# Kernel tuning notes

Measured on AMD Instinct MI355X. Metric: run time of the kernel, lower is better.

The kernel has to match this reference:

```python
import jax, jax.numpy as jnp
import numpy as np

B, S, D = 4, 1024, 768
H = 12
DK = D // H            # 64
NUM_EMB = 10
MAX_DIST = 100000.0 * 2 ** 0.5
POS_SCALE = 100000.0   # tile positions live in [0, 100000]


def setup_inputs() -> dict:
    key = jax.random.key(0)
    ks = jax.random.split(key, 12)
    query = jax.random.normal(ks[0], (B, S, D), dtype=jnp.float32)
    key_t = jax.random.normal(ks[1], (B, S, D), dtype=jnp.float32)
    value = jax.random.normal(ks[2], (B, S, D), dtype=jnp.float32)
    tile_positions = jax.random.uniform(ks[3], (B, S, 2), dtype=jnp.float32) * POS_SCALE
    # Linear weights, torch layout [out, in]; xavier_uniform init, zero bias
    lim = float(np.sqrt(6.0 / (D + D)))
    Wq = jax.random.uniform(ks[4], (D, D), minval=-lim, maxval=lim, dtype=jnp.float32)
    Wk = jax.random.uniform(ks[5], (D, D), minval=-lim, maxval=lim, dtype=jnp.float32)
    Wv = jax.random.uniform(ks[6], (D, D), minval=-lim, maxval=lim, dtype=jnp.float32)
    bq = jnp.zeros((D,), jnp.float32)
    bk = jnp.zeros((D,), jnp.float32)
    bv = jnp.zeros((D,), jnp.float32)
    emb_k = jax.random.normal(ks[7], (NUM_EMB, DK), dtype=jnp.float32)  # nn.Embedding default N(0,1)
    return {"query": query, "key": key_t, "value": value,
            "tile_positions": tile_positions,
            "Wq": Wq, "bq": bq, "Wk": Wk, "bk": bk, "Wv": Wv, "bv": bv,
            "emb_k": emb_k}


def reference(query, key, value, tile_positions, Wq, bq, Wk, bk, Wv, bv, emb_k):
    b, s, _ = query.shape
    # projections -> [B, H, S, DK]
    q = (query @ Wq.T + bq).reshape(b, s, H, DK).transpose(0, 2, 1, 3)
    k = (key   @ Wk.T + bk).reshape(b, s, H, DK).transpose(0, 2, 1, 3)
    v = (value @ Wv.T + bv).reshape(b, s, H, DK).transpose(0, 2, 1, 3)
    # pairwise distances, normalized, discretized to embedding indices
    pos = jax.lax.stop_gradient(tile_positions)
    diff = pos[:, :, None, :] - pos[:, None, :, :]          # [B,S,S,2]
    dist = jnp.sqrt(jnp.sum(diff * diff, axis=-1)) / MAX_DIST  # [B,S,S]
    idx = jnp.clip(jnp.round(dist * (NUM_EMB - 1)), 0, NUM_EMB - 1).astype(jnp.int32)
    rk = emb_k[idx]                                          # [B,S,S,DK]
    # logits: QK^T plus distance-aware key bias
    attn_logits = jnp.einsum('bhqd,bhkd->bhqk', q, k)
    attn_logits = attn_logits + jnp.einsum('bhqd,bqkd->bhqk', q, rk)
    attn_logits = attn_logits / (DK ** 0.5)
    attention = jax.nn.softmax(attn_logits, axis=-1)
    out = jnp.einsum('bhqk,bhkd->bhqd', attention, v)       # [B,H,S,DK]
    out = out.transpose(0, 2, 1, 3).reshape(b, s, -1)       # [B,S,D]
    return out
```

## Files before the change

### kernel.cpp

```cpp
#include <hip/hip_runtime.h>
#include <hip/hip_bf16.h>

#define Bsz 4
#define Ssz 1024
#define Dsz 768
#define Hn 12
#define DKsz 64
#define NUMEMB 10

#define IDX_OFF 64
#define K_OFF   4194368
#define V_OFF   10485824
#define WBF_OFF 16777280
#define XBF_OFF 20316224
#define WS_TIER_B 20316224ULL
#define WS_TIER_A 39190592ULL

#define NXz 3145728
#define NWz 589824

#define QE_RS 12
#define QE_QS 776

typedef __attribute__((ext_vector_type(8))) short short8;
typedef __attribute__((ext_vector_type(8))) float float8;
typedef __attribute__((ext_vector_type(4))) float f32x4;
typedef __attribute__((ext_vector_type(4))) unsigned int u32x4;
typedef __attribute__((ext_vector_type(2))) unsigned int u32x2;
typedef __attribute__((ext_vector_type(4))) short s16x4;

__device__ __forceinline__ float bfbits2f(short u) {
    union { unsigned int i; float f; } v;
    v.i = ((unsigned int)(unsigned short)u) << 16;
    return v.f;
}
__device__ __forceinline__ unsigned short f2bf_bits(float f) {
    __hip_bfloat16 h = __float2bfloat16(f);
    return *reinterpret_cast<unsigned short*>(&h);
}

__device__ __forceinline__ void gld16(const short* g, short* l) {
    __builtin_amdgcn_global_load_lds(
        (const __attribute__((address_space(1))) void*)g,
        (__attribute__((address_space(3))) void*)l, 16, 0, 0);
}

template<bool BF16>
__device__ __forceinline__ float loadf(const void* base, size_t idx) {
    if constexpr (BF16) return __bfloat162float(((const __hip_bfloat16*)base)[idx]);
    else return ((const float*)base)[idx];
}
template<bool BF16>
__device__ __forceinline__ short8 load8bf(const void* base, size_t idx) {
    if constexpr (BF16) {
        return *(const short8*)((const short*)base + idx);
    } else {
        float8 f = *(const float8*)((const float*)base + idx);
        short8 r;
#pragma unroll
        for (int i = 0; i < 8; i++) r[i] = (short)f2bf_bits(f[i]);
        return r;
    }
}
template<bool BF16>
__device__ __forceinline__ float8 load8f(const void* base, size_t idx) {
    if constexpr (BF16) {
        short8 s = *(const short8*)((const short*)base + idx);
        float8 f;
#pragma unroll
        for (int i = 0; i < 8; i++) f[i] = bfbits2f(s[i]);
        return f;
    } else {
        return *(const float8*)((const float*)base + idx);
    }
}

__global__ __launch_bounds__(64) void detect_kernel(
    const unsigned int* __restrict__ q, const unsigned int* __restrict__ p,
    const unsigned int* __restrict__ w, const unsigned int* __restrict__ e,
    int* __restrict__ flags)
{
    const int which = blockIdx.x;
    const unsigned int* ptr = (which == 0) ? q : ((which == 1) ? p : ((which == 2) ? w : e));
    const int n = (which == 3) ? 320 : ((which == 1) ? 4096 : 1024);
    int cnt = 0;
    for (int i = threadIdx.x; i < n; i += 64) {
        const unsigned int ex = (ptr[i] >> 7) & 0xFF;
        cnt += (ex >= 110 && ex <= 145) ? 1 : 0;
    }
#pragma unroll
    for (int off = 1; off < 64; off <<= 1) cnt += __shfl_xor(cnt, off, 64);
    if (threadIdx.x == 0) flags[which] = (2 * cnt > n) ? 1 : 0;
}

__global__ __launch_bounds__(256) void conv_kernel(
    const void* __restrict__ X0, const void* __restrict__ X1, const void* __restrict__ X2,
    const void* __restrict__ W0, const void* __restrict__ W1, const void* __restrict__ W2,
    const int* __restrict__ flags, short* __restrict__ Xbf, short* __restrict__ Wbf,
    int doX)
{
    const long t = (long)blockIdx.x * 256 + threadIdx.x;
    const bool xb = flags[0] != 0, wb = flags[2] != 0;
    if (doX) {
        const long i8 = t * 8;
        if (i8 < (long)3 * NXz) {
            const int z = (int)(i8 / NXz);
            const long off = i8 - (long)z * NXz;
            const void* X = (z == 0) ? X0 : ((z == 1) ? X1 : X2);
            short8 v = xb ? load8bf<true>(X, off) : load8bf<false>(X, off);
            *(short8*)(Xbf + i8) = v;
        } else {
            const long j = i8 - (long)3 * NXz;
            const int z = (int)(j / NWz);
            const long off = j - (long)z * NWz;
            const void* W = (z == 0) ? W0 : ((z == 1) ? W1 : W2);
            short8 v = wb ? load8bf<true>(W, off) : load8bf<false>(W, off);
            *(short8*)(Wbf + j) = v;
        }
    } else {
        const long j = t * 8;
        const int z = (int)(j / NWz);
        const long off = j - (long)z * NWz;
        const void* W = (z == 0) ? W0 : ((z == 1) ? W1 : W2);
        short8 v = wb ? load8bf<true>(W, off) : load8bf<false>(W, off);
        *(short8*)(Wbf + j) = v;
    }
}

template<bool PB>
__device__ __forceinline__ void idx_body(
    const void* pos, unsigned char* __restrict__ idxb)
{
    const int kt = blockIdx.x, qt = blockIdx.y, b = blockIdx.z;
    const int t = threadIdx.x;
    const int r = t >> 2, cc = t & 3;
    const int q = qt * 64 + r;
    const float qx = loadf<PB>(pos, ((size_t)b * Ssz + q) * 2);
    const float qy = loadf<PB>(pos, ((size_t)b * Ssz + q) * 2 + 1);
    const float MAXD = 141421.35623730951f;
    const int k0 = kt * 64 + cc * 16;
    unsigned int w[4];
#pragma unroll
    for (int g = 0; g < 4; g++) {
        unsigned int acc = 0;
#pragma unroll
        for (int u = 0; u < 4; u++) {
            const int k = k0 + g * 4 + u;
            const float kx = loadf<PB>(pos, ((size_t)b * Ssz + k) * 2);
            const float ky = loadf<PB>(pos, ((size_t)b * Ssz + k) * 2 + 1);
            const float dx = __fsub_rn(qx, kx);
            const float dy = __fsub_rn(qy, ky);
            const float ss = __fadd_rn(__fmul_rn(dx, dx), __fmul_rn(dy, dy));
            const float dist = __fdiv_rn(sqrtf(ss), MAXD);
            const float d9 = __fmul_rn(dist, 9.0f);
            int idx = (int)rintf(d9);
            idx = idx < 0 ? 0 : (idx > NUMEMB - 1 ? NUMEMB - 1 : idx);
            acc |= ((unsigned int)idx) << (8 * u);
        }
        w[g] = acc;
    }
    u32x4 v; v[0] = w[0]; v[1] = w[1]; v[2] = w[2]; v[3] = w[3];
    *(u32x4*)(idxb + ((size_t)(b * Ssz + q)) * Ssz + k0) = v;
}

__global__ __launch_bounds__(256) void idx_kernel(
    const void* pos, const int* __restrict__ flags, unsigned char* __restrict__ idxb)
{
    if (flags[1] != 0) idx_body<true >(pos, idxb);
    else               idx_body<false>(pos, idxb);
}

__device__ __forceinline__ void proj_epilogue(
    f32x4 (&acc)[2][4], const void* bias, bool biasbf, void* Y, bool ybf,
    int zmode, int m0, int n0, int wm, int wn, int l15, int quad)
{
#pragma unroll
    for (int j = 0; j < 4; j++) {
        const int n = n0 + wn * 64 + j * 16 + l15;
        const float bv_ = biasbf ? loadf<true>(bias, n) : loadf<false>(bias, n);
        const int hh = n >> 6, dk = n & 63;
#pragma unroll
        for (int i = 0; i < 2; i++) {
            const int ms = m0 + wm * 32 + i * 16 + quad * 4;
            const int bb = ms >> 10;
            const int s0 = ms & 1023;
            if (zmode == 2) {
                s16x4 pkv;
#pragma unroll
                for (int r = 0; r < 4; r++) pkv[r] = (short)f2bf_bits(acc[i][j][r] + bv_);
                *(s16x4*)((short*)Y + (((size_t)bb * Hn + hh) * DKsz + dk) * Ssz + s0) = pkv;
            } else if (zmode == 1) {
#pragma unroll
                for (int r = 0; r < 4; r++)
                    ((__hip_bfloat16*)Y)[(((size_t)bb * Hn + hh) * Ssz + (s0 + r)) * DKsz + dk] =
                        __float2bfloat16(acc[i][j][r] + bv_);
            } else {
#pragma unroll
                for (int r = 0; r < 4; r++) {
                    const float val = acc[i][j][r] + bv_;
                    const size_t oi = (size_t)(ms + r) * Dsz + n;
                    if (ybf) ((__hip_bfloat16*)Y)[oi] = __float2bfloat16(val);
                    else     ((float*)Y)[oi] = val;
                }
            }
        }
    }
}

template<bool XB, bool WB>
__device__ __forceinline__ void proj_body(
    const void* X, const void* W, const void* bias, bool biasbf, void* Y, bool ybf,
    int zmode, int bx, int by, short* As, short* Bs)
{
    const int tid  = threadIdx.x;
    const int wave = tid >> 6;
    const int lane = tid & 63;
    const int l15  = lane & 15;
    const int quad = lane >> 4;
    const int wm = wave & 1;
    const int wn = wave >> 1;
    const int m0 = bx * 64;
    const int n0 = by * 128;

    f32x4 acc[2][4];
#pragma unroll
    for (int i = 0; i < 2; i++)
#pragma unroll
        for (int j = 0; j < 4; j++) acc[i][j] = (f32x4)0.0f;

    const int r0 = tid >> 3;
    const int cc = tid & 7;

    short8 pa0 = load8bf<XB>(X, (size_t)(m0 + r0)      * Dsz + cc * 8);
    short8 pa1 = load8bf<XB>(X, (size_t)(m0 + 32 + r0) * Dsz + cc * 8);
    short8 pb0 = load8bf<WB>(W, (size_t)(n0 + r0)      * Dsz + cc * 8);
    short8 pb1 = load8bf<WB>(W, (size_t)(n0 + 32 + r0) * Dsz + cc * 8);
    short8 pb2 = load8bf<WB>(W, (size_t)(n0 + 64 + r0) * Dsz + cc * 8);
    short8 pb3 = load8bf<WB>(W, (size_t)(n0 + 96 + r0) * Dsz + cc * 8);

    for (int kk = 0; kk < Dsz; kk += 64) {
        __syncthreads();
        *(short8*)&As[(r0)      * 72 + cc * 8] = pa0;
        *(short8*)&As[(32 + r0) * 72 + cc * 8] = pa1;
        *(short8*)&Bs[(r0)      * 72 + cc * 8] = pb0;
        *(short8*)&Bs[(32 + r0) * 72 + cc * 8] = pb1;
        *(short8*)&Bs[(64 + r0) * 72 + cc * 8] = pb2;
        *(short8*)&Bs[(96 + r0) * 72 + cc * 8] = pb3;
        __syncthreads();

        if (kk + 64 < Dsz) {
            const int k2 = kk + 64 + cc * 8;
            pa0 = load8bf<XB>(X, (size_t)(m0 + r0)      * Dsz + k2);
            pa1 = load8bf<XB>(X, (size_t)(m0 + 32 + r0) * Dsz + k2);
            pb0 = load8bf<WB>(W, (size_t)(n0 + r0)      * Dsz + k2);
            pb1 = load8bf<WB>(W, (size_t)(n0 + 32 + r0) * Dsz + k2);
            pb2 = load8bf<WB>(W, (size_t)(n0 + 64 + r0) * Dsz + k2);
            pb3 = load8bf<WB>(W, (size_t)(n0 + 96 + r0) * Dsz + k2);
        }

#pragma unroll
        for (int st = 0; st < 2; st++) {
            short8 af[2], bf[4];
#pragma unroll
            for (int i = 0; i < 2; i++)
                af[i] = *(const short8*)&As[(wm * 32 + i * 16 + l15) * 72 + st * 32 + quad * 8];
#pragma unroll
            for (int j = 0; j < 4; j++)
                bf[j] = *(const short8*)&Bs[(wn * 64 + j * 16 + l15) * 72 + st * 32 + quad * 8];
#pragma unroll
            for (int i = 0; i < 2; i++)
#pragma unroll
                for (int j = 0; j < 4; j++)
                    acc[i][j] = __builtin_amdgcn_mfma_f32_16x16x32_bf16(af[i], bf[j], acc[i][j], 0, 0, 0);
        }
    }
    proj_epilogue(acc, bias, biasbf, Y, ybf, zmode, m0, n0, wm, wn, l15, quad);
}

__global__ __launch_bounds__(256) void proj_kernel(
    const void* X0, const void* X1, const void* X2,
    const void* Wq, const void* bq, const void* Wk, const void* bk,
    const void* Wv, const void* bv,
    void* Qw, void* Kw, void* Vw, const int* __restrict__ flags,
    int fx, int fw)
{
    __shared__ __align__(16) short As[64 * 72];
    __shared__ __align__(16) short Bs[128 * 72];
    const int z = blockIdx.z;
    const void* X = (z == 0) ? X0 : ((z == 1) ? X1 : X2);
    const void* W = (z == 0) ? Wq : ((z == 1) ? Wk : Wv);
    const void* B = (z == 0) ? bq : ((z == 1) ? bk : bv);
    void* Y = (z == 0) ? Qw : ((z == 1) ? Kw : Vw);
    const bool xb = fx || flags[0] != 0;
    const bool wb = fw || flags[2] != 0;
    const bool biasbf = flags[2] != 0;
    const bool ybf = (flags[0] != 0) || (z != 0);
    if (xb) { if (wb) proj_body<true , true >(X, W, B, biasbf, Y, ybf, z, blockIdx.x, blockIdx.y, As, Bs);
              else    proj_body<true , false>(X, W, B, biasbf, Y, ybf, z, blockIdx.x, blockIdx.y, As, Bs); }
    else    { if (wb) proj_body<false, true >(X, W, B, biasbf, Y, ybf, z, blockIdx.x, blockIdx.y, As, Bs);
              else    proj_body<false, false>(X, W, B, biasbf, Y, ybf, z, blockIdx.x, blockIdx.y, As, Bs); }
}

__global__ __launch_bounds__(256) void proj_lds_kernel(
    const short* __restrict__ Xbf, const short* __restrict__ Wbf,
    const void* bq, const void* bk, const void* bv,
    void* Qw, void* Kw, void* Vw, const int* __restrict__ flags)
{
    __shared__ __align__(16) short As[2][64 * 64];
    __shared__ __align__(16) short Bs[2][128 * 64];

    const int z = blockIdx.z;
    const short* X = Xbf + (size_t)z * NXz;
    const short* W = Wbf + (size_t)z * NWz;
    const void* Bp = (z == 0) ? bq : ((z == 1) ? bk : bv);
    void* Y = (z == 0) ? Qw : ((z == 1) ? Kw : Vw);
    const bool biasbf = flags[2] != 0;
    const bool ybf = (flags[0] != 0) || (z != 0);

    const int tid  = threadIdx.x;
    const int wave = tid >> 6;
    const int lane = tid & 63;
    const int l15  = lane & 15;
    const int quad = lane >> 4;
    const int wm = wave & 1;
    const int wn = wave >> 1;
    const int m0 = blockIdx.x * 64;
    const int n0 = blockIdx.y * 128;

    f32x4 acc[2][4];
#pragma unroll
    for (int i = 0; i < 2; i++)
#pragma unroll
        for (int j = 0; j < 4; j++) acc[i][j] = (f32x4)0.0f;

    const int sr = lane >> 3;
    const int sc = lane & 7;
    const int gch = (sc ^ sr) * 8;

    const short* ga = X + (size_t)(m0 + wave * 16 + sr) * Dsz + gch;
    const short* gb = W + (size_t)(n0 + wave * 32 + sr) * Dsz + gch;

    auto STAGE = [&](int bb, int kk) {
        const short* gA = ga + kk;
        gld16(gA,            &As[bb][(wave * 16     ) * 64]);
        gld16(gA + 8 * Dsz,  &As[bb][(wave * 16 + 8 ) * 64]);
        const short* gB = gb + kk;
        gld16(gB,            &Bs[bb][(wave * 32     ) * 64]);
        gld16(gB + 8 * Dsz,  &Bs[bb][(wave * 32 + 8 ) * 64]);
        gld16(gB + 16 * Dsz, &Bs[bb][(wave * 32 + 16) * 64]);
        gld16(gB + 24 * Dsz, &Bs[bb][(wave * 32 + 24) * 64]);
    };

    STAGE(0, 0);
    asm volatile("s_waitcnt vmcnt(0)" ::: "memory");
    __builtin_amdgcn_s_barrier();

    for (int t = 0; t < 12; ++t) {
        const int cb = t & 1;
        if (t + 1 < 12) STAGE(cb ^ 1, (t + 1) * 64);

#pragma unroll
        for (int st = 0; st < 2; st++) {
            const int slot = ((st * 4 + quad) ^ (l15 & 7)) * 8;
            short8 af[2], bf[4];
#pragma unroll
            for (int i = 0; i < 2; i++)
                af[i] = *(const short8*)&As[cb][(wm * 32 + i * 16 + l15) * 64 + slot];
#pragma unroll
            for (int j = 0; j < 4; j++)
                bf[j] = *(const short8*)&Bs[cb][(wn * 64 + j * 16 + l15) * 64 + slot];
#pragma unroll
            for (int i = 0; i < 2; i++)
#pragma unroll
                for (int j = 0; j < 4; j++)
                    acc[i][j] = __builtin_amdgcn_mfma_f32_16x16x32_bf16(af[i], bf[j], acc[i][j], 0, 0, 0);
        }

        asm volatile("s_waitcnt vmcnt(0)" ::: "memory");
        __builtin_amdgcn_s_barrier();
    }
    proj_epilogue(acc, Bp, biasbf, Y, ybf, z, m0, n0, wm, wn, l15, quad);
}

template<bool QB, bool EB>
__device__ __forceinline__ void attn_body(
    const void* Qw, const short* __restrict__ Ks, const short* __restrict__ Vs,
    const unsigned char* __restrict__ idxb, const void* __restrict__ emb, void* out,
    unsigned short* Klds, unsigned short* Vtlds, float* qe)
{
    const int qt = blockIdx.x, h = blockIdx.y, b = blockIdx.z;
    const int tid  = threadIdx.x;
    const int wave = tid >> 6;
    const int lane = tid & 63;
    const int l15  = lane & 15;
    const int quad = lane >> 4;

    const float CSC = 0.18033688011112042f;

    for (int p = tid; p < 64 * NUMEMB; p += 256) {
        const int row = p / NUMEMB, e = p - row * NUMEMB;
        const size_t qoff = ((size_t)b * Ssz + qt * 64 + row) * Dsz + h * DKsz;
        float s = 0.f;
#pragma unroll
        for (int c = 0; c < 8; c++) {
            short8 qv = load8bf<QB>(Qw, qoff + c * 8);
            float8 ef = load8f<EB>(emb, (size_t)e * DKsz + c * 8);
#pragma unroll
            for (int i = 0; i < 8; i++) s += bfbits2f(qv[i]) * ef[i];
        }
        const float val = s * CSC;
#pragma unroll
        for (int qd = 0; qd < 4; qd++) qe[qd * QE_QS + row * QE_RS + e] = val;
    }

    short8 qfrag[2];
    {
        const size_t qbase = ((size_t)b * Ssz + qt * 64 + wave * 16 + l15) * Dsz + h * DKsz;
        qfrag[0] = load8bf<QB>(Qw, qbase + quad * 8);
        qfrag[1] = load8bf<QB>(Qw, qbase + 32 + quad * 8);
    }

    float m_run = -1e30f, l_run = 0.f;
    f32x4 oacc[4];
#pragma unroll
    for (int j = 0; j < 4; j++) oacc[j] = (f32x4)0.0f;

    const int r0 = tid >> 3, cc = tid & 7;
    const int ksl = (cc + 4 * (r0 & 1) - r0) & 7;
    const int kwoff = r0 * 72 + ksl * 8;
    const int vwoff = r0 * 72 + cc * 8;

    int koff[4][2];
#pragma unroll
    for (int jb = 0; jb < 4; jb++) {
        const int krow = (jb & 2) * 16 + (l15 >> 2) * 8 + (jb & 1) * 4 + (l15 & 3);
        const int base = quad + 4 * (l15 & 1) - (l15 & 3) + 8;
#pragma unroll
        for (int st = 0; st < 2; st++)
            koff[jb][st] = krow * 72 + ((base + 4 * (st ^ (jb & 1))) & 7) * 8;
    }

    const short* kp = Ks + ((size_t)(b * Hn + h) * Ssz) * DKsz + tid * 8;
    const short* vp = Vs + ((size_t)(b * Hn + h) * DKsz + r0) * Ssz + cc * 8;
    const unsigned char* ip = idxb + ((size_t)b * Ssz + qt * 64 + wave * 16 + l15) * Ssz + quad * 8;
    const float* qeL = qe + quad * QE_QS + (wave * 16 + l15) * QE_RS;

    short8 pk0 = *(const short8*)(kp);
    short8 pk1 = *(const short8*)(kp + 2048);
    short8 pv0 = *(const short8*)(vp);
    short8 pv1 = *(const short8*)(vp + 32 * Ssz);
    u32x2 idA = *(const u32x2*)(ip);
    u32x2 idB = *(const u32x2*)(ip + 32);

    *(short8*)&Klds[kwoff]            = pk0;
    *(short8*)&Klds[32 * 72 + kwoff]  = pk1;
    *(short8*)&Vtlds[vwoff]           = pv0;
    *(short8*)&Vtlds[32 * 72 + vwoff] = pv1;
    __syncthreads();

    for (int it = 0; it < 16; ++it) {
        const int cur = (it & 1) ? (64 * 72) : 0;
        const int nxt = (it & 1) ? 0 : (64 * 72);
        const unsigned int jd[4] = { idA[0], idA[1], idB[0], idB[1] };

        if (it + 1 < 16) {
            kp += 4096;
            vp += 64;
            ip += 64;
            pk0 = *(const short8*)(kp);
            pk1 = *(const short8*)(kp + 2048);
            pv0 = *(const short8*)(vp);
            pv1 = *(const short8*)(vp + 32 * Ssz);
            idA = *(const u32x2*)(ip);
            idB = *(const u32x2*)(ip + 32);
        }

        f32x4 sf[4];
#pragma unroll
        for (int jb = 0; jb < 4; jb++) sf[jb] = (f32x4)0.0f;
        __builtin_amdgcn_s_setprio(1);
#pragma unroll
        for (int st = 0; st < 2; st++) {
#pragma unroll
            for (int jb = 0; jb < 4; jb++) {
                short8 kf = *(const short8*)&Klds[cur + koff[jb][st]];
                sf[jb] = __builtin_amdgcn_mfma_f32_16x16x32_bf16(kf, qfrag[st], sf[jb], 0, 0, 0);
            }
        }
        __builtin_amdgcn_s_setprio(0);

        float sv[4][4];
#pragma unroll
        for (int jb = 0; jb < 4; jb++) {
            const unsigned int iw = jd[jb];
#pragma unroll
            for (int r = 0; r < 4; r++)
                sv[jb][r] = fmaf(sf[jb][r], CSC, qeL[(iw >> (8 * r)) & 0xFF]);
        }

        float t0 = fmaxf(fmaxf(sv[0][0], sv[0][1]), fmaxf(sv[0][2], sv[0][3]));
        float t1 = fmaxf(fmaxf(sv[1][0], sv[1][1]), fmaxf(sv[1][2], sv[1][3]));
        float t2 = fmaxf(fmaxf(sv[2][0], sv[2][1]), fmaxf(sv[2][2], sv[2][3]));
        float t3 = fmaxf(fmaxf(sv[3][0], sv[3][1]), fmaxf(sv[3][2], sv[3][3]));
        float vmax = fmaxf(fmaxf(t0, t1), fmaxf(t2, t3));
        vmax = fmaxf(vmax, __shfl_xor(vmax, 16, 64));
        vmax = fmaxf(vmax, __shfl_xor(vmax, 32, 64));

        if (!__all(vmax - m_run <= 8.0f)) {
            const float mnew = fmaxf(m_run, vmax);
            const float alpha = exp2f(m_run - mnew);
            m_run = mnew;
            l_run *= alpha;
            float aO[4];
#pragma unroll
            for (int r = 0; r < 4; r++)
                aO[r] = __shfl(alpha, (lane & 48) | (quad * 4 + r), 64);
#pragma unroll
            for (int j = 0; j < 4; j++) {
                f32x4 o = oacc[j];
#pragma unroll
                for (int r = 0; r < 4; r++) o[r] *= aO[r];
                oacc[j] = o;
            }
        }

#pragma unroll
        for (int jb = 0; jb < 4; jb++)
#pragma unroll
            for (int r = 0; r < 4; r++)
                sv[jb][r] = exp2f(sv[jb][r] - m_run);

        float s0 = (sv[0][0] + sv[0][1]) + (sv[0][2] + sv[0][3]);
        float s1 = (sv[1][0] + sv[1][1]) + (sv[1][2] + sv[1][3]);
        float s2 = (sv[2][0] + sv[2][1]) + (sv[2][2] + sv[2][3]);
        float s3 = (sv[3][0] + sv[3][1]) + (sv[3][2] + sv[3][3]);
        float psum = (s0 + s1) + (s2 + s3);
        psum += __shfl_xor(psum, 16, 64);
        psum += __shfl_xor(psum, 32, 64);
        l_run += psum;

        short8 pa[2];
#pragma unroll
        for (int st = 0; st < 2; st++)
#pragma unroll
            for (int j = 0; j < 8; j++)
                pa[st][j] = (short)f2bf_bits(sv[2 * st + (j >> 2)][j & 3]);

        __builtin_amdgcn_s_setprio(1);
#pragma unroll
        for (int st = 0; st < 2; st++) {
#pragma unroll
            for (int j = 0; j < 4; j++) {
                short8 vb = *(const short8*)&Vtlds[cur + (j * 16 + l15) * 72 + st * 32 + quad * 8];
                oacc[j] = __builtin_amdgcn_mfma_f32_16x16x32_bf16(pa[st], vb, oacc[j], 0, 0, 0);
            }
        }
        __builtin_amdgcn_s_setprio(0);

        if (it + 1 < 16) {
            *(short8*)&Klds[nxt + kwoff]            = pk0;
            *(short8*)&Klds[nxt + 32 * 72 + kwoff]  = pk1;
            *(short8*)&Vtlds[nxt + vwoff]           = pv0;
            *(short8*)&Vtlds[nxt + 32 * 72 + vwoff] = pv1;
        }
        __syncthreads();
    }

    const float inv = 1.0f / l_run;
    float invO[4];
#pragma unroll
    for (int r = 0; r < 4; r++)
        invO[r] = __shfl(inv, (lane & 48) | (quad * 4 + r), 64);

#pragma unroll
    for (int r = 0; r < 4; r++) {
        const int m = qt * 64 + wave * 16 + quad * 4 + r;
#pragma unroll
        for (int j = 0; j < 4; j++) {
            const int n = h * DKsz + j * 16 + l15;
            const float val = oacc[j][r] * invO[r];
            const size_t oidx = ((size_t)b * Ssz + m) * Dsz + n;
            if constexpr (QB) ((__hip_bfloat16*)out)[oidx] = __float2bfloat16(val);
            else              ((float*)out)[oidx] = val;
        }
    }
}

__global__ __launch_bounds__(256) void attn_kernel(
    const void* Qw, const short* __restrict__ Ks, const short* __restrict__ Vs,
    const unsigned char* __restrict__ idxb, const void* __restrict__ emb, void* out,
    const int* __restrict__ flags)
{
    __shared__ __align__(16) unsigned short Klds[2 * 64 * 72];
    __shared__ __align__(16) unsigned short Vtlds[2 * 64 * 72];
    __shared__ __align__(16) float qe[4 * QE_QS];

    const bool qb = flags[0] != 0, eb = flags[3] != 0;
    if (qb) { if (eb) attn_body<true , true >(Qw, Ks, Vs, idxb, emb, out, Klds, Vtlds, qe);
              else    attn_body<true , false>(Qw, Ks, Vs, idxb, emb, out, Klds, Vtlds, qe); }
    else    { if (eb) attn_body<false, true >(Qw, Ks, Vs, idxb, emb, out, Klds, Vtlds, qe);
              else    attn_body<false, false>(Qw, Ks, Vs, idxb, emb, out, Klds, Vtlds, qe); }
}

extern "C" void kernel_launch(void* const* d_in, const int* in_sizes, int n_in,
                              void* d_out, int out_size, void* d_ws, size_t ws_size,
                              hipStream_t stream) {
    const void* query = d_in[0];
    const void* key   = d_in[1];
    const void* value = d_in[2];
    const void* tpos  = d_in[3];
    const void* Wq    = d_in[4];
    const void* bq    = d_in[5];
    const void* Wk    = d_in[6];
    const void* bk    = d_in[7];
    const void* Wv    = d_in[8];
    const void* bv    = d_in[9];
    const void* emb   = d_in[10];

    int*           flags = (int*)d_ws;
    unsigned char* idxb  = (unsigned char*)d_ws + IDX_OFF;
    void*          Kw    = (char*)d_ws + K_OFF;
    void*          Vw    = (char*)d_ws + V_OFF;
    short*         Wbf   = (short*)((char*)d_ws + WBF_OFF);
    short*         Xbf   = (short*)((char*)d_ws + XBF_OFF);
    void*          Qw    = d_out;

    const bool tierA = ws_size >= WS_TIER_A;
    const bool tierB = !tierA && ws_size >= WS_TIER_B;

    detect_kernel<<<4, 64, 0, stream>>>(
        (const unsigned int*)query, (const unsigned int*)tpos,
        (const unsigned int*)Wq, (const unsigned int*)emb, flags);

    if (tierA)
        conv_kernel<<<5472, 256, 0, stream>>>(query, key, value, Wq, Wk, Wv, flags, Xbf, Wbf, 1);
    else if (tierB)
        conv_kernel<<<864, 256, 0, stream>>>(query, key, value, Wq, Wk, Wv, flags, Xbf, Wbf, 0);

    idx_kernel<<<dim3(16, 16, Bsz), 256, 0, stream>>>(tpos, flags, idxb);

    if (tierA)
        proj_lds_kernel<<<dim3(64, 6, 3), 256, 0, stream>>>(
            Xbf, Wbf, bq, bk, bv, Qw, Kw, Vw, flags);
    else if (tierB)
        proj_kernel<<<dim3(64, 6, 3), 256, 0, stream>>>(
            query, key, value,
            Wbf, bq, Wbf + NWz, bk, Wbf + 2 * NWz, bv,
            Qw, Kw, Vw, flags, 0, 1);
    else
        proj_kernel<<<dim3(64, 6, 3), 256, 0, stream>>>(
            query, key, value, Wq, bq, Wk, bk, Wv, bv,
            Qw, Kw, Vw, flags, 0, 0);

    attn_kernel<<<dim3(16, Hn, Bsz), 256, 0, stream>>>(
        Qw, (const short*)Kw, (const short*)Vw, idxb, emb, d_out, flags);
}
```

Measured before the change: 211.8 us.

## Fold dtype detection into conv, enlarge projection tile, shrink qe LDS table

```diff
diff --git a/kernel.cpp b/kernel.cpp
--- a/kernel.cpp
+++ b/kernel.cpp
@@ -19,9 +19,6 @@
 #define NXz 3145728
 #define NWz 589824
 
-#define QE_RS 12
-#define QE_QS 776
-
 typedef __attribute__((ext_vector_type(8))) short short8;
 typedef __attribute__((ext_vector_type(8))) float float8;
 typedef __attribute__((ext_vector_type(4))) float f32x4;
@@ -43,6 +40,17 @@
     __builtin_amdgcn_global_load_lds(
         (const __attribute__((address_space(1))) void*)g,
         (__attribute__((address_space(3))) void*)l, 16, 0, 0);
+}
+
+__device__ __forceinline__ int dtvote(const unsigned int* p, int n) {
+    int cnt = 0;
+    for (int i = (threadIdx.x & 63); i < n; i += 64) {
+        const unsigned int ex = (p[i] >> 7) & 0xFF;
+        cnt += (ex >= 110 && ex <= 145) ? 1 : 0;
+    }
+#pragma unroll
+    for (int off = 1; off < 64; off <<= 1) cnt += __shfl_xor(cnt, off, 64);
+    return (2 * cnt > n) ? 1 : 0;
 }
 
 template<bool BF16>
@@ -83,24 +91,29 @@
     const int which = blockIdx.x;
     const unsigned int* ptr = (which == 0) ? q : ((which == 1) ? p : ((which == 2) ? w : e));
     const int n = (which == 3) ? 320 : ((which == 1) ? 4096 : 1024);
-    int cnt = 0;
-    for (int i = threadIdx.x; i < n; i += 64) {
-        const unsigned int ex = (ptr[i] >> 7) & 0xFF;
-        cnt += (ex >= 110 && ex <= 145) ? 1 : 0;
-    }
-#pragma unroll
-    for (int off = 1; off < 64; off <<= 1) cnt += __shfl_xor(cnt, off, 64);
-    if (threadIdx.x == 0) flags[which] = (2 * cnt > n) ? 1 : 0;
+    const int f = dtvote(ptr, n);
+    if (threadIdx.x == 0) flags[which] = f;
 }
 
 __global__ __launch_bounds__(256) void conv_kernel(
     const void* __restrict__ X0, const void* __restrict__ X1, const void* __restrict__ X2,
     const void* __restrict__ W0, const void* __restrict__ W1, const void* __restrict__ W2,
-    const int* __restrict__ flags, short* __restrict__ Xbf, short* __restrict__ Wbf,
+    const void* __restrict__ tpos, const void* __restrict__ emb,
+    int* __restrict__ flags, short* __restrict__ Xbf, short* __restrict__ Wbf,
     int doX)
 {
+    if (blockIdx.x == 1) {
+        const int f = dtvote((const unsigned int*)tpos, 1024);
+        if (threadIdx.x == 0) flags[1] = f;
+    } else if (blockIdx.x == 3) {
+        const int f = dtvote((const unsigned int*)emb, 320);
+        if (threadIdx.x == 0) flags[3] = f;
+    }
+    const bool xb = dtvote((const unsigned int*)X0, 256) != 0;
+    const bool wb = dtvote((const unsigned int*)W0, 256) != 0;
+    if (blockIdx.x == 0 && threadIdx.x == 0) { flags[0] = xb ? 1 : 0; flags[2] = wb ? 1 : 0; }
+
     const long t = (long)blockIdx.x * 256 + threadIdx.x;
-    const bool xb = flags[0] != 0, wb = flags[2] != 0;
     if (doX) {
         const long i8 = t * 8;
         if (i8 < (long)3 * NXz) {
@@ -301,12 +314,12 @@
               else    proj_body<false, false>(X, W, B, biasbf, Y, ybf, z, blockIdx.x, blockIdx.y, As, Bs); }
 }
 
-__global__ __launch_bounds__(256) void proj_lds_kernel(
+__global__ __launch_bounds__(256) void proj128_kernel(
     const short* __restrict__ Xbf, const short* __restrict__ Wbf,
     const void* bq, const void* bk, const void* bv,
     void* Qw, void* Kw, void* Vw, const int* __restrict__ flags)
 {
-    __shared__ __align__(16) short As[2][64 * 64];
+    __shared__ __align__(16) short As[2][128 * 64];
     __shared__ __align__(16) short Bs[2][128 * 64];
 
     const int z = blockIdx.z;
@@ -324,35 +337,31 @@
     const int quad = lane >> 4;
     const int wm = wave & 1;
     const int wn = wave >> 1;
-    const int m0 = blockIdx.x * 64;
+    const int m0 = blockIdx.x * 128;
     const int n0 = blockIdx.y * 128;
 
-    f32x4 acc[2][4];
-#pragma unroll
-    for (int i = 0; i < 2; i++)
+    f32x4 acc[4][4];
+#pragma unroll
+    for (int i = 0; i < 4; i++)
 #pragma unroll
         for (int j = 0; j < 4; j++) acc[i][j] = (f32x4)0.0f;
 
     const int sr = lane >> 3;
     const int sc = lane & 7;
-    const int gch = (sc ^ sr) * 8;
-
-    const short* ga = X + (size_t)(m0 + wave * 16 + sr) * Dsz + gch;
-    const short* gb = W + (size_t)(n0 + wave * 32 + sr) * Dsz + gch;
+    const short* gaL = X + (size_t)(m0 + wave * 32 + sr) * Dsz + (sc ^ sr) * 8;
+    const short* gbL = W + (size_t)(n0 + wave * 32 + sr) * Dsz + (sc ^ sr) * 8;
 
     auto STAGE = [&](int bb, int kk) {
-        const short* gA = ga + kk;
-        gld16(gA,            &As[bb][(wave * 16     ) * 64]);
-        gld16(gA + 8 * Dsz,  &As[bb][(wave * 16 + 8 ) * 64]);
-        const short* gB = gb + kk;
-        gld16(gB,            &Bs[bb][(wave * 32     ) * 64]);
-        gld16(gB + 8 * Dsz,  &Bs[bb][(wave * 32 + 8 ) * 64]);
-        gld16(gB + 16 * Dsz, &Bs[bb][(wave * 32 + 16) * 64]);
-        gld16(gB + 24 * Dsz, &Bs[bb][(wave * 32 + 24) * 64]);
+#pragma unroll
+        for (int r = 0; r < 4; r++) {
+            gld16(gaL + (size_t)r * 8 * Dsz + kk, &As[bb][(wave * 32 + r * 8) * 64]);
+            gld16(gbL + (size_t)r * 8 * Dsz + kk, &Bs[bb][(wave * 32 + r * 8) * 64]);
+        }
     };
 
     STAGE(0, 0);
     asm volatile("s_waitcnt vmcnt(0)" ::: "memory");
+    __builtin_amdgcn_sched_barrier(0);
     __builtin_amdgcn_s_barrier();
 
     for (int t = 0; t < 12; ++t) {
@@ -362,24 +371,56 @@
 #pragma unroll
         for (int st = 0; st < 2; st++) {
             const int slot = ((st * 4 + quad) ^ (l15 & 7)) * 8;
-            short8 af[2], bf[4];
-#pragma unroll
-            for (int i = 0; i < 2; i++)
-                af[i] = *(const short8*)&As[cb][(wm * 32 + i * 16 + l15) * 64 + slot];
+            short8 af[4], bf[4];
+#pragma unroll
+            for (int i = 0; i < 4; i++)
+                af[i] = *(const short8*)&As[cb][(wm * 64 + i * 16 + l15) * 64 + slot];
 #pragma unroll
             for (int j = 0; j < 4; j++)
                 bf[j] = *(const short8*)&Bs[cb][(wn * 64 + j * 16 + l15) * 64 + slot];
 #pragma unroll
-            for (int i = 0; i < 2; i++)
+            for (int i = 0; i < 4; i++)
 #pragma unroll
                 for (int j = 0; j < 4; j++)
                     acc[i][j] = __builtin_amdgcn_mfma_f32_16x16x32_bf16(af[i], bf[j], acc[i][j], 0, 0, 0);
         }
 
         asm volatile("s_waitcnt vmcnt(0)" ::: "memory");
+        __builtin_amdgcn_sched_barrier(0);
         __builtin_amdgcn_s_barrier();
     }
-    proj_epilogue(acc, Bp, biasbf, Y, ybf, z, m0, n0, wm, wn, l15, quad);
+
+#pragma unroll
+    for (int j = 0; j < 4; j++) {
+        const int n = n0 + wn * 64 + j * 16 + l15;
+        const float bv_ = biasbf ? loadf<true>(Bp, n) : loadf<false>(Bp, n);
+        const int hh = n >> 6, dk = n & 63;
+#pragma unroll
+        for (int i = 0; i < 4; i++) {
+            const int ms = m0 + wm * 64 + i * 16 + quad * 4;
+            const int bb = ms >> 10;
+            const int s0 = ms & 1023;
+            if (z == 2) {
+                s16x4 pkv;
+#pragma unroll
+                for (int r = 0; r < 4; r++) pkv[r] = (short)f2bf_bits(acc[i][j][r] + bv_);
+                *(s16x4*)((short*)Y + (((size_t)bb * Hn + hh) * DKsz + dk) * Ssz + s0) = pkv;
+            } else if (z == 1) {
+#pragma unroll
+                for (int r = 0; r < 4; r++)
+                    ((__hip_bfloat16*)Y)[(((size_t)bb * Hn + hh) * Ssz + (s0 + r)) * DKsz + dk] =
+                        __float2bfloat16(acc[i][j][r] + bv_);
+            } else {
+#pragma unroll
+                for (int r = 0; r < 4; r++) {
+                    const float val = acc[i][j][r] + bv_;
+                    const size_t oi = (size_t)(ms + r) * Dsz + n;
+                    if (ybf) ((__hip_bfloat16*)Y)[oi] = __float2bfloat16(val);
+                    else     ((float*)Y)[oi] = val;
+                }
+            }
+        }
+    }
 }
 
 template<bool QB, bool EB>
@@ -408,9 +449,7 @@
 #pragma unroll
             for (int i = 0; i < 8; i++) s += bfbits2f(qv[i]) * ef[i];
         }
-        const float val = s * CSC;
-#pragma unroll
-        for (int qd = 0; qd < 4; qd++) qe[qd * QE_QS + row * QE_RS + e] = val;
+        qe[p] = s * CSC;
     }
 
     short8 qfrag[2];
@@ -443,7 +482,7 @@
     const short* kp = Ks + ((size_t)(b * Hn + h) * Ssz) * DKsz + tid * 8;
     const short* vp = Vs + ((size_t)(b * Hn + h) * DKsz + r0) * Ssz + cc * 8;
     const unsigned char* ip = idxb + ((size_t)b * Ssz + qt * 64 + wave * 16 + l15) * Ssz + quad * 8;
-    const float* qeL = qe + quad * QE_QS + (wave * 16 + l15) * QE_RS;
+    const int qrow10 = (wave * 16 + l15) * NUMEMB;
 
     short8 pk0 = *(const short8*)(kp);
     short8 pk1 = *(const short8*)(kp + 2048);
@@ -495,7 +534,7 @@
             const unsigned int iw = jd[jb];
 #pragma unroll
             for (int r = 0; r < 4; r++)
-                sv[jb][r] = fmaf(sf[jb][r], CSC, qeL[(iw >> (8 * r)) & 0xFF]);
+                sv[jb][r] = fmaf(sf[jb][r], CSC, qe[qrow10 + ((iw >> (8 * r)) & 0xFF)]);
         }
 
         float t0 = fmaxf(fmaxf(sv[0][0], sv[0][1]), fmaxf(sv[0][2], sv[0][3]));
@@ -593,7 +632,7 @@
 {
     __shared__ __align__(16) unsigned short Klds[2 * 64 * 72];
     __shared__ __align__(16) unsigned short Vtlds[2 * 64 * 72];
-    __shared__ __align__(16) float qe[4 * QE_QS];
+    __shared__ __align__(16) float qe[64 * NUMEMB];
 
     const bool qb = flags[0] != 0, eb = flags[3] != 0;
     if (qb) { if (eb) attn_body<true , true >(Qw, Ks, Vs, idxb, emb, out, Klds, Vtlds, qe);
@@ -628,29 +667,29 @@
     const bool tierA = ws_size >= WS_TIER_A;
     const bool tierB = !tierA && ws_size >= WS_TIER_B;
 
-    detect_kernel<<<4, 64, 0, stream>>>(
-        (const unsigned int*)query, (const unsigned int*)tpos,
-        (const unsigned int*)Wq, (const unsigned int*)emb, flags);
-
-    if (tierA)
-        conv_kernel<<<5472, 256, 0, stream>>>(query, key, value, Wq, Wk, Wv, flags, Xbf, Wbf, 1);
-    else if (tierB)
-        conv_kernel<<<864, 256, 0, stream>>>(query, key, value, Wq, Wk, Wv, flags, Xbf, Wbf, 0);
-
-    idx_kernel<<<dim3(16, 16, Bsz), 256, 0, stream>>>(tpos, flags, idxb);
-
-    if (tierA)
-        proj_lds_kernel<<<dim3(64, 6, 3), 256, 0, stream>>>(
+    if (tierA) {
+        conv_kernel<<<5472, 256, 0, stream>>>(query, key, value, Wq, Wk, Wv,
+                                              tpos, emb, flags, Xbf, Wbf, 1);
+        idx_kernel<<<dim3(16, 16, Bsz), 256, 0, stream>>>(tpos, flags, idxb);
+        proj128_kernel<<<dim3(32, 6, 3), 256, 0, stream>>>(
             Xbf, Wbf, bq, bk, bv, Qw, Kw, Vw, flags);
-    else if (tierB)
+    } else if (tierB) {
+        conv_kernel<<<864, 256, 0, stream>>>(query, key, value, Wq, Wk, Wv,
+                                             tpos, emb, flags, Xbf, Wbf, 0);
+        idx_kernel<<<dim3(16, 16, Bsz), 256, 0, stream>>>(tpos, flags, idxb);
         proj_kernel<<<dim3(64, 6, 3), 256, 0, stream>>>(
             query, key, value,
             Wbf, bq, Wbf + NWz, bk, Wbf + 2 * NWz, bv,
             Qw, Kw, Vw, flags, 0, 1);
-    else
+    } else {
+        detect_kernel<<<4, 64, 0, stream>>>(
+            (const unsigned int*)query, (const unsigned int*)tpos,
+            (const unsigned int*)Wq, (const unsigned int*)emb, flags);
+        idx_kernel<<<dim3(16, 16, Bsz), 256, 0, stream>>>(tpos, flags, idxb);
         proj_kernel<<<dim3(64, 6, 3), 256, 0, stream>>>(
             query, key, value, Wq, bq, Wk, bk, Wv, bv,
             Qw, Kw, Vw, flags, 0, 0);
+    }
 
     attn_kernel<<<dim3(16, Hn, Bsz), 256, 0, stream>>>(
         Qw, (const short*)Kw, (const short*)Vw, idxb, emb, d_out, flags);
```

New measurement: 212.7 us. About the same (+0.5%).
